# Kernel tuning notes

Hardware: AMD Instinct MI355X
Metric: run time of the kernel (lower is better)

## Reference

```python
import jax, jax.numpy as jnp
import numpy as np

T_STEPS = 10       # T_pos = T_neg = 10 hardcoded in forward
ATTN_SCALE = 0.125 # scale hardcoded in forward (not head_dim**-0.5)
V_TH = 1.0         # spikingjelly IFNode defaults: v_threshold=1.0, v_reset=0.0 (hard reset)
SG_ALPHA = 4.0     # default Sigmoid surrogate alpha

@jax.custom_vjp
def spike(v):
    return (v >= 0.0).astype(v.dtype)

def _spike_fwd(v):
    return spike(v), v

def _spike_bwd(v, g):
    sg = jax.nn.sigmoid(SG_ALPHA * v)
    return (g * SG_ALPHA * sg * (1.0 - sg),)

spike.defvjp(_spike_fwd, _spike_bwd)

def if_node_const_input(y, T=T_STEPS):
    """Multi-step IF neuron driven by the SAME input y at every step.
    charge: v += y; fire: s = H(v - 1); hard reset: v = (1 - s) * v.
    Returns spikes of shape [T, *y.shape]."""
    def step(v, _):
        v = v + y
        s = spike(v - V_TH)
        v = (1.0 - s) * v
        return v, s
    _, spikes = jax.lax.scan(step, jnp.zeros_like(y), None, length=T)
    return spikes

def setup_inputs() -> dict:
    key = jax.random.key(0)
    ks = jax.random.split(key, 6)
    N, C = 2048, 2048
    x = jax.random.normal(ks[0], (N, C), dtype=jnp.float32)
    freqs_cis = jax.random.normal(ks[1], (N, 64), dtype=jnp.float32)  # unused by forward
    w_scale = 0.02
    wq = jax.random.normal(ks[2], (C, C), dtype=jnp.float32) * w_scale
    wk = jax.random.normal(ks[3], (C, C), dtype=jnp.float32) * w_scale
    wv = jax.random.normal(ks[4], (C, C), dtype=jnp.float32) * w_scale
    wo = jax.random.normal(ks[5], (C, C), dtype=jnp.float32) * w_scale
    return {"x": x, "freqs_cis": freqs_cis, "wq": wq, "wk": wk, "wv": wv, "wo": wo}

def reference(x, freqs_cis, wq, wk, wv, wo):
    N, C = x.shape
    n_heads, head_dim = 16, 128  # C == n_heads * head_dim; n_kv_heads == n_heads so repeat_kv is a no-op
    T = T_STEPS

    x_pos = jax.nn.relu(x)
    x_neg = jax.nn.relu(-x)

    # Input is identical at every timestep, so apply the linear once, then run IF over T.
    def branch(xb):
        q = if_node_const_input(xb @ wq)  # [T, N, C] binary spikes
        k = if_node_const_input(xb @ wk)
        v = if_node_const_input(xb @ wv)
        return q, k, v

    qp, kp, vp = branch(x_pos)
    qn, kn, vn = branch(x_neg)
    xq = (qp - qn).reshape(T, N, n_heads, head_dim)
    xk = (kp - kn).reshape(T, N, n_heads, head_dim)
    xv = (vp - vn).reshape(T, N, n_heads, head_dim)

    # no-softmax attention over the HEAD axis, per token: [T,N,H,H]
    attn = jnp.einsum('tnhd,tnmd->tnhm', xq, xk) * ATTN_SCALE
    x_attn = jnp.einsum('tnhm,tnmd->tnhd', attn, xv)          # [T,N,H,Dh]
    x_attn = jnp.swapaxes(x_attn, -1, -2).reshape(T, N, C)    # transpose(-1,-2) then merge

    xo = x_attn @ wo  # [T, N, C]
    return xo.mean(axis=0)
```

## Files before the change

kernel.cpp:

```cpp
#include <hip/hip_runtime.h>
#include <hip/hip_bf16.h>


#define LIST_CAP (512u * 1024u)
#define FLAG_EPS 4e-4f

typedef __attribute__((ext_vector_type(8))) short short8;
typedef __attribute__((ext_vector_type(16))) float floatx16;

__device__ const unsigned d_LUT[16] = {0u, 0x3FFu, 0x2AAu, 0x124u, 0x88u,
                                       0x210u, 0x20u, 0x40u, 0x80u, 0x100u,
                                       0x200u, 0u, 0u, 0u, 0u, 0u};

__device__ __forceinline__ void bf16x2_rne(float a, unsigned& p1, unsigned& p2) {
  const unsigned u = __float_as_uint(a);
  const unsigned t1 = u + 0x7FFFu + ((u >> 16) & 1u);
  p1 = t1 >> 16;
  const float r = a - __uint_as_float(t1 & 0xFFFF0000u);
  const unsigned u2 = __float_as_uint(r);
  p2 = (u2 + 0x7FFFu + ((u2 >> 16) & 1u)) >> 16;
}

template <int ZERO_CNT, int FRAG>
__global__ __launch_bounds__(256) void wsplit(
    const float* __restrict__ W0, const float* __restrict__ W1,
    const float* __restrict__ W2, unsigned short* __restrict__ Bpk,
    int NCT, unsigned* __restrict__ cnt) {
  if (ZERO_CNT && blockIdx.x == 0 && blockIdx.y == 0 && threadIdx.x == 0)
    *cnt = 0u;
  __shared__ float Wf[32 * 132];
  const int ct = blockIdx.x, k0 = blockIdx.y * 32;
  const int c0 = ct * 128;
  const int sel = c0 >> 11;
  const float* W = (sel == 0) ? W0 : ((sel == 1) ? W1 : W2);
  const int cc0 = c0 & 2047;
  const int t = threadIdx.x;

  const int kr = t >> 3, cq = (t & 7) * 16;
#pragma unroll
  for (int u = 0; u < 4; u++) {
    const float4 v = *(const float4*)(W + (size_t)(k0 + kr) * 2048 + cc0 + cq + 4 * u);
    *(float4*)&Wf[kr * 132 + cq + 4 * u] = v;
  }
  __syncthreads();

  const int cc = t >> 1, ch0 = (t & 1) * 2;
  if (FRAG) {
    unsigned short* base = Bpk + ((size_t)((ct >> 1) * 64 + blockIdx.y)) * 16384 +
                           (size_t)(ct & 1) * 8192;
#pragma unroll
    for (int c = ch0; c < ch0 + 2; c++) {
      unsigned q1[8], q2[8];
#pragma unroll
      for (int e = 0; e < 8; e++) bf16x2_rne(Wf[(c * 8 + e) * 132 + cc], q1[e], q2[e]);
      const int ks = c >> 1, kh = c & 1;
      const int off1 = ((0 * 2 + ks) * 4 + (cc >> 5)) * 512 + (kh * 32 + (cc & 31)) * 8;
      const int off2 = ((1 * 2 + ks) * 4 + (cc >> 5)) * 512 + (kh * 32 + (cc & 31)) * 8;
      uint4 P1, P2;
      P1.x = q1[0] | (q1[1] << 16); P1.y = q1[2] | (q1[3] << 16);
      P1.z = q1[4] | (q1[5] << 16); P1.w = q1[6] | (q1[7] << 16);
      P2.x = q2[0] | (q2[1] << 16); P2.y = q2[2] | (q2[3] << 16);
      P2.z = q2[4] | (q2[5] << 16); P2.w = q2[6] | (q2[7] << 16);
      *(uint4*)&base[off1] = P1;
      *(uint4*)&base[off2] = P2;
    }
  } else {
    unsigned short* img1 = Bpk + ((size_t)(0 * NCT + ct) * 64 + blockIdx.y) * 4096;
    unsigned short* img2 = Bpk + ((size_t)(1 * NCT + ct) * 64 + blockIdx.y) * 4096;
#pragma unroll
    for (int c = ch0; c < ch0 + 2; c++) {
      unsigned q1[8], q2[8];
#pragma unroll
      for (int e = 0; e < 8; e++) bf16x2_rne(Wf[(c * 8 + e) * 132 + cc], q1[e], q2[e]);
      const int off = cc * 32 + 8 * (c ^ ((cc >> 1) & 3));
      uint4 P1, P2;
      P1.x = q1[0] | (q1[1] << 16); P1.y = q1[2] | (q1[3] << 16);
      P1.z = q1[4] | (q1[5] << 16); P1.w = q1[6] | (q1[7] << 16);
      P2.x = q2[0] | (q2[1] << 16); P2.y = q2[2] | (q2[3] << 16);
      P2.z = q2[4] | (q2[5] << 16); P2.w = q2[6] | (q2[7] << 16);
      *(uint4*)&img1[off] = P1;
      *(uint4*)&img2[off] = P2;
    }
  }
}

template <int RELU, int FRAG>
__global__ __launch_bounds__(256) void asplit(
    const float* __restrict__ src, unsigned short* __restrict__ Apk, int NRT) {
  const int rt = blockIdx.x, k0i = blockIdx.y;
  const int t = threadIdx.x;
  const int r = t >> 1, half = t & 1;
  int grow = rt * 128 + r;
  float sgn = 1.f;
  if (RELU && grow >= 2048) { grow -= 2048; sgn = -1.f; }
  const float* s = src + (size_t)grow * 2048 + k0i * 32 + half * 16;
  float f[16];
#pragma unroll
  for (int u = 0; u < 4; u++) {
    const float4 v = *(const float4*)(s + 4 * u);
    f[4 * u + 0] = v.x; f[4 * u + 1] = v.y;
    f[4 * u + 2] = v.z; f[4 * u + 3] = v.w;
  }
  if (RELU) {
#pragma unroll
    for (int e = 0; e < 16; e++) f[e] = fmaxf(sgn * f[e], 0.f);
  }
  unsigned q1[16], q2[16];
#pragma unroll
  for (int e = 0; e < 16; e++) bf16x2_rne(f[e], q1[e], q2[e]);

  if (FRAG) {
    unsigned short* base = Apk + ((size_t)((rt >> 1) * 64 + k0i)) * 16384 +
                           (size_t)(rt & 1) * 8192;
#pragma unroll
    for (int cc = 0; cc < 2; cc++) {
      const int c = half * 2 + cc;
      const int ks = c >> 1, kh = c & 1;
      const int off1 = ((0 * 2 + ks) * 4 + (r >> 5)) * 512 + (kh * 32 + (r & 31)) * 8;
      const int off2 = ((1 * 2 + ks) * 4 + (r >> 5)) * 512 + (kh * 32 + (r & 31)) * 8;
      const int e0 = cc * 8;
      uint4 P1, P2;
      P1.x = q1[e0 + 0] | (q1[e0 + 1] << 16); P1.y = q1[e0 + 2] | (q1[e0 + 3] << 16);
      P1.z = q1[e0 + 4] | (q1[e0 + 5] << 16); P1.w = q1[e0 + 6] | (q1[e0 + 7] << 16);
      P2.x = q2[e0 + 0] | (q2[e0 + 1] << 16); P2.y = q2[e0 + 2] | (q2[e0 + 3] << 16);
      P2.z = q2[e0 + 4] | (q2[e0 + 5] << 16); P2.w = q2[e0 + 6] | (q2[e0 + 7] << 16);
      *(uint4*)&base[off1] = P1;
      *(uint4*)&base[off2] = P2;
    }
  } else {
    unsigned short* img1 = Apk + ((size_t)(0 * NRT + rt) * 64 + k0i) * 4096;
    unsigned short* img2 = Apk + ((size_t)(1 * NRT + rt) * 64 + k0i) * 4096;
#pragma unroll
    for (int cc = 0; cc < 2; cc++) {
      const int c = half * 2 + cc;
      const int off = r * 32 + 8 * (c ^ ((r >> 1) & 3));
      const int e0 = cc * 8;
      uint4 P1, P2;
      P1.x = q1[e0 + 0] | (q1[e0 + 1] << 16); P1.y = q1[e0 + 2] | (q1[e0 + 3] << 16);
      P1.z = q1[e0 + 4] | (q1[e0 + 5] << 16); P1.w = q1[e0 + 6] | (q1[e0 + 7] << 16);
      P2.x = q2[e0 + 0] | (q2[e0 + 1] << 16); P2.y = q2[e0 + 2] | (q2[e0 + 3] << 16);
      P2.z = q2[e0 + 4] | (q2[e0 + 5] << 16); P2.w = q2[e0 + 6] | (q2[e0 + 7] << 16);
      *(uint4*)&img1[off] = P1;
      *(uint4*)&img2[off] = P2;
    }
  }
}

__global__ __launch_bounds__(512, 2) void gemm256(
    const unsigned short* __restrict__ Apk, const unsigned short* __restrict__ Bpk,
    unsigned char* __restrict__ MaskJ, unsigned* __restrict__ list,
    unsigned* __restrict__ cnt) {
  __shared__ unsigned short lds[2][4][8192];

  const int tid = threadIdx.x;
  const int wave = tid >> 6, lane = tid & 63;
  const int lm = lane & 31, lg = lane >> 5;
  const int wr = wave >> 2, wc = wave & 3;

  const int orig = (int)blockIdx.x;
  const int wg = (orig & 7) * 48 + (orig >> 3);
  const int bx = wg % 24, by = wg / 24;

  const unsigned short* Aimg = Apk + (size_t)by * 64 * 16384;
  const unsigned short* Bimg = Bpk + (size_t)bx * 64 * 16384;

  auto issue2 = [&](int kt, int nb, int c) {
    const unsigned short* g = ((c < 2) ? (Aimg + (size_t)c * 8192)
                                       : (Bimg + (size_t)(c - 2) * 8192)) +
                              (size_t)kt * 16384;
#pragma unroll
    for (int rr = 0; rr < 2; rr++)
      __builtin_amdgcn_global_load_lds(
          (const __attribute__((address_space(1))) unsigned*)(g + rr * 4096 + tid * 8),
          (__attribute__((address_space(3))) unsigned*)(&lds[nb][c][rr * 4096 + wave * 512]),
          16, 0, 0);
  };

  floatx16 acc[4][2];
#pragma unroll
  for (int i = 0; i < 4; i++)
#pragma unroll
    for (int j = 0; j < 2; j++)
#pragma unroll
      for (int e = 0; e < 16; e++) acc[i][j][e] = 0.f;

#pragma unroll
  for (int c = 0; c < 4; c++) issue2(0, 0, c);
  asm volatile("s_waitcnt vmcnt(0)" ::: "memory");
  __builtin_amdgcn_s_barrier();
  __builtin_amdgcn_sched_barrier(0);

  const int rt0 = 2 * (wc & 1);
  for (int kt = 0; kt < 64; kt++) {
    const int cur = kt & 1, nxt = cur ^ 1;
    const unsigned short* Ab = &lds[cur][wr][0];
    const unsigned short* Bb = &lds[cur][2 + (wc >> 1)][0];
#pragma unroll
    for (int ks = 0; ks < 2; ks++) {
      short8 a1[4], a2[4];
#pragma unroll
      for (int it = 0; it < 4; it++) {
        a1[it] = *(const short8*)&Ab[((0 * 2 + ks) * 4 + it) * 512 + lane * 8];
        a2[it] = *(const short8*)&Ab[((1 * 2 + ks) * 4 + it) * 512 + lane * 8];
      }
#pragma unroll
      for (int jt = 0; jt < 2; jt++) {
        const short8 b1 = *(const short8*)&Bb[((0 * 2 + ks) * 4 + rt0 + jt) * 512 + lane * 8];
        const short8 b2 = *(const short8*)&Bb[((1 * 2 + ks) * 4 + rt0 + jt) * 512 + lane * 8];
        if (ks == 0 && kt < 63) {
          issue2(kt + 1, nxt, jt * 2 + 0);
          issue2(kt + 1, nxt, jt * 2 + 1);
        }
        __builtin_amdgcn_s_barrier();
        __builtin_amdgcn_s_setprio(1);
#pragma unroll
        for (int it = 0; it < 4; it++)
          acc[it][jt] = __builtin_amdgcn_mfma_f32_32x32x16_bf16(a1[it], b1, acc[it][jt], 0, 0, 0);
#pragma unroll
        for (int it = 0; it < 4; it++)
          acc[it][jt] = __builtin_amdgcn_mfma_f32_32x32x16_bf16(a1[it], b2, acc[it][jt], 0, 0, 0);
#pragma unroll
        for (int it = 0; it < 4; it++)
          acc[it][jt] = __builtin_amdgcn_mfma_f32_32x32x16_bf16(a2[it], b1, acc[it][jt], 0, 0, 0);
        __builtin_amdgcn_s_setprio(0);
        if (ks == 1 && jt == 1)
          asm volatile("s_waitcnt vmcnt(0)" ::: "memory");
        __builtin_amdgcn_s_barrier();
      }
    }
    __builtin_amdgcn_sched_barrier(0);
  }

#pragma unroll
  for (int it = 0; it < 4; it++) {
#pragma unroll
    for (int jt = 0; jt < 2; jt++) {
      const int gn = bx * 256 + 64 * wc + 32 * jt + lm;
#pragma unroll
      for (int reg = 0; reg < 16; reg++) {
        const int gm = by * 256 + 128 * wr + 32 * it + (reg & 3) + 8 * (reg >> 2) + 4 * lg;
        const float y = acc[it][jt][reg];
        float r = __builtin_amdgcn_rcpf(y);
        r = fminf(fmaxf(r, -1.0f), 12.0f);
        const float jf = floorf(r);
        const float d0 = fmaf(jf, y, -1.0f);
        const float i0 = fminf(fmaxf(jf, 1.0f), 10.0f);
        const float i1 = fminf(fmaxf(jf + 1.0f, 1.0f), 10.0f);
        const float e0 = fmaf(i0, y, -1.0f);
        const float e1 = fmaf(i1, y, -1.0f);
        const float mind = fminf(fabsf(e0), fabsf(e1));
        const unsigned J = (unsigned)(int)((d0 >= 0.0f) ? jf : jf + 1.0f);
        MaskJ[(size_t)gm * 6144 + gn] = (unsigned char)((J <= 10u) ? J : 0u);
        if (mind < FLAG_EPS) {
          const unsigned idx = atomicAdd(cnt, 1u);
          if (idx < LIST_CAP) list[idx] = ((unsigned)gm << 13) | (unsigned)gn;
        }
      }
    }
  }
}

template <int MODE>
__global__ __launch_bounds__(256, 4) void gemm_dma(
    const unsigned short* __restrict__ Apk, const unsigned short* __restrict__ Bpk,
    int NRT, int NCT, unsigned char* __restrict__ MaskJ,
    unsigned* __restrict__ list, unsigned* __restrict__ cnt,
    float* __restrict__ Out) {
  __shared__ unsigned short sh[4][4096];

  const int tid = threadIdx.x;
  const int bx = blockIdx.x, by = blockIdx.y;
  const int lane = tid & 63, wave = tid >> 6;
  const int wr = wave >> 1, wc = wave & 1;
  const int lm = lane & 31, lg = lane >> 5;

  const unsigned short* gsrc =
      (wave < 2) ? (Apk + ((size_t)(wave * NRT + by) * 64) * 4096)
                 : (Bpk + ((size_t)((wave - 2) * NCT + bx) * 64) * 4096);

  floatx16 acc[2][2];
#pragma unroll
  for (int i = 0; i < 2; i++)
#pragma unroll
    for (int j = 0; j < 2; j++)
#pragma unroll
      for (int e = 0; e < 16; e++) acc[i][j][e] = 0.f;

  for (int k0i = 0; k0i < 64; k0i++) {
    __syncthreads();
    const unsigned short* gp = gsrc + (size_t)k0i * 4096;
#pragma unroll
    for (int i = 0; i < 8; i++) {
      __builtin_amdgcn_global_load_lds(
          (const __attribute__((address_space(1))) unsigned*)(gp + i * 512 + lane * 8),
          (__attribute__((address_space(3))) unsigned*)(&sh[wave][i * 512]), 16, 0, 0);
    }
    __syncthreads();

#pragma unroll
    for (int ks = 0; ks < 2; ks++) {
      const int ch = ks * 2 + lg;
      short8 a1[2], a2[2], b1[2], b2[2];
#pragma unroll
      for (int it = 0; it < 2; it++) {
        const int row = 64 * wr + 32 * it + lm;
        const int off = row * 32 + 8 * (ch ^ ((row >> 1) & 3));
        a1[it] = *(const short8*)&sh[0][off];
        a2[it] = *(const short8*)&sh[1][off];
      }
#pragma unroll
      for (int jt = 0; jt < 2; jt++) {
        const int row = 64 * wc + 32 * jt + lm;
        const int off = row * 32 + 8 * (ch ^ ((row >> 1) & 3));
        b1[jt] = *(const short8*)&sh[2][off];
        b2[jt] = *(const short8*)&sh[3][off];
      }
#pragma unroll
      for (int it = 0; it < 2; it++)
#pragma unroll
        for (int jt = 0; jt < 2; jt++)
          acc[it][jt] = __builtin_amdgcn_mfma_f32_32x32x16_bf16(
              a1[it], b1[jt], acc[it][jt], 0, 0, 0);
#pragma unroll
      for (int it = 0; it < 2; it++)
#pragma unroll
        for (int jt = 0; jt < 2; jt++)
          acc[it][jt] = __builtin_amdgcn_mfma_f32_32x32x16_bf16(
              a1[it], b2[jt], acc[it][jt], 0, 0, 0);
#pragma unroll
      for (int it = 0; it < 2; it++)
#pragma unroll
        for (int jt = 0; jt < 2; jt++)
          acc[it][jt] = __builtin_amdgcn_mfma_f32_32x32x16_bf16(
              a2[it], b1[jt], acc[it][jt], 0, 0, 0);
    }
  }

#pragma unroll
  for (int it = 0; it < 2; it++) {
#pragma unroll
    for (int jt = 0; jt < 2; jt++) {
      const int gn = bx * 128 + 64 * wc + 32 * jt + lm;
#pragma unroll
      for (int reg = 0; reg < 16; reg++) {
        const int gm = by * 128 + 64 * wr + 32 * it + (reg & 3) + 8 * (reg >> 2) + 4 * lg;
        const float y = acc[it][jt][reg];
        if (MODE == 1) {
          Out[(size_t)gm * 2048 + gn] = y * 0.1f;
        } else {
          float r = __builtin_amdgcn_rcpf(y);
          r = fminf(fmaxf(r, -1.0f), 12.0f);
          const float jf = floorf(r);
          const float d0 = fmaf(jf, y, -1.0f);
          const float i0 = fminf(fmaxf(jf, 1.0f), 10.0f);
          const float i1 = fminf(fmaxf(jf + 1.0f, 1.0f), 10.0f);
          const float e0 = fmaf(i0, y, -1.0f);
          const float e1 = fmaf(i1, y, -1.0f);
          const float mind = fminf(fabsf(e0), fabsf(e1));
          const unsigned J = (unsigned)(int)((d0 >= 0.0f) ? jf : jf + 1.0f);
          MaskJ[(size_t)gm * 6144 + gn] = (unsigned char)((J <= 10u) ? J : 0u);
          if (mind < FLAG_EPS) {
            const unsigned idx = atomicAdd(cnt, 1u);
            if (idx < LIST_CAP) list[idx] = ((unsigned)gm << 13) | (unsigned)gn;
          }
        }
      }
    }
  }
}

__global__ __launch_bounds__(256) void transpose_w(
    const float* __restrict__ W0, const float* __restrict__ W1,
    const float* __restrict__ W2, float* __restrict__ WT) {
  __shared__ float tile[32][33];
  const int k0 = blockIdx.x * 32;
  const int c0 = blockIdx.y * 32;
  const int sel = c0 >> 11;
  const float* W = (sel == 0) ? W0 : ((sel == 1) ? W1 : W2);
  const int cc0 = c0 & 2047;
  const int tx = threadIdx.x, ty = threadIdx.y;
#pragma unroll
  for (int rep = 0; rep < 4; rep++)
    tile[ty + 8 * rep][tx] = W[(size_t)(k0 + ty + 8 * rep) * 2048 + cc0 + tx];
  __syncthreads();
#pragma unroll
  for (int rep = 0; rep < 4; rep++)
    WT[(size_t)(c0 + ty + 8 * rep) * 2048 + k0 + tx] = tile[tx][ty + 8 * rep];
}

__global__ __launch_bounds__(256) void rescue(
    const float* __restrict__ X, const float* __restrict__ WT,
    const unsigned* __restrict__ list, const unsigned* __restrict__ cnt,
    unsigned char* __restrict__ MaskJ) {
  const unsigned nItems = min(*cnt, LIST_CAP);
  const unsigned gtid = blockIdx.x * blockDim.x + threadIdx.x;
  const unsigned wave = gtid >> 6, lane = gtid & 63;
  const unsigned nWaves = (gridDim.x * blockDim.x) >> 6;

  for (unsigned i = wave; i < nItems; i += nWaves) {
    const unsigned e = list[i];
    const int r = (int)(e >> 13), c = (int)(e & 8191u);
    const float* xrow = X + (size_t)((r < 2048) ? r : r - 2048) * 2048;
    const float sg = (r < 2048) ? 1.f : -1.f;
    const float* wrow = WT + (size_t)c * 2048;
    double s = 0.0;
#pragma unroll
    for (int it = 0; it < 8; it++) {
      const int k = (it * 64 + (int)lane) * 4;
      const float4 xv = *(const float4*)(xrow + k);
      const float4 wv = *(const float4*)(wrow + k);
      const float a0 = fmaxf(sg * xv.x, 0.f);
      const float a1 = fmaxf(sg * xv.y, 0.f);
      const float a2 = fmaxf(sg * xv.z, 0.f);
      const float a3 = fmaxf(sg * xv.w, 0.f);
      s += (double)a0 * (double)wv.x + (double)a1 * (double)wv.y +
           (double)a2 * (double)wv.z + (double)a3 * (double)wv.w;
    }
#pragma unroll
    for (int off = 32; off > 0; off >>= 1) s += __shfl_down(s, off);
    if (lane == 0) {
      double v = 0.0;
      unsigned J = 0;
#pragma unroll
      for (int t = 0; t < 10; t++) {
        v += s;
        if (J == 0u && v >= 1.0) J = (unsigned)(t + 1);
      }
      MaskJ[(size_t)r * 6144 + c] = (unsigned char)J;
    }
  }
}

__global__ __launch_bounds__(256) void spike_attn(const unsigned char* __restrict__ MaskJ,
                                                  float* __restrict__ xbar) {
  const int n = blockIdx.x;
  const int tid = threadIdx.x;
  const int lane = tid & 63;

  __shared__ unsigned long long qpB[16][2], qnB[16][2], kpB[16][2], knB[16][2];
  __shared__ float xvT[16 * 132];
  __shared__ float attnS[16 * 17];
  __shared__ unsigned lutS[16];

  if (tid < 16) lutS[tid] = d_LUT[tid];
  __syncthreads();

  const unsigned char* mp = MaskJ + (size_t)n * 6144;
  const unsigned char* mn = MaskJ + (size_t)(n + 2048) * 6144;

  unsigned q_p[8], q_n[8], k_p[8], k_n[8], v_p[8], v_n[8];
#pragma unroll
  for (int j = 0; j < 8; j++) {
    const int c = tid + 256 * j;
    q_p[j] = lutS[mp[c]];        q_n[j] = lutS[mn[c]];
    k_p[j] = lutS[mp[2048 + c]]; k_n[j] = lutS[mn[2048 + c]];
    v_p[j] = lutS[mp[4096 + c]]; v_n[j] = lutS[mn[4096 + c]];
  }

  float acc[8];
#pragma unroll
  for (int j = 0; j < 8; j++) acc[j] = 0.f;

  for (int t = 0; t < 10; t++) {
#pragma unroll
    for (int j = 0; j < 8; j++) {
      const int c = tid + 256 * j;
      const unsigned long long bqp = __ballot((q_p[j] >> t) & 1u);
      const unsigned long long bqn = __ballot((q_n[j] >> t) & 1u);
      const unsigned long long bkp = __ballot((k_p[j] >> t) & 1u);
      const unsigned long long bkn = __ballot((k_n[j] >> t) & 1u);
      const int h = c >> 7, word = (c >> 6) & 1;
      if (lane == 0) {
        qpB[h][word] = bqp; qnB[h][word] = bqn;
        kpB[h][word] = bkp; knB[h][word] = bkn;
      }
      const int m = h, d = c & 127;
      xvT[m * 132 + d] =
          (float)((v_p[j] >> t) & 1u) - (float)((v_n[j] >> t) & 1u);
    }
    __syncthreads();

    {
      const int h = tid >> 4, m = tid & 15;
      int dot = 0;
#pragma unroll
      for (int w = 0; w < 2; w++) {
        const unsigned long long qp = qpB[h][w], qn = qnB[h][w];
        const unsigned long long kp = kpB[m][w], kn = knB[m][w];
        dot += __popcll(qp & kp) + __popcll(qn & kn) -
               __popcll(qp & kn) - __popcll(qn & kp);
      }
      attnS[h * 17 + m] = (float)dot * 0.125f;
    }
    __syncthreads();

    {
      const int h = tid & 15;
      float arow[16];
#pragma unroll
      for (int m = 0; m < 16; m++) arow[m] = attnS[h * 17 + m];
#pragma unroll
      for (int j = 0; j < 8; j++) {
        const int d = (tid + 256 * j) >> 4;
        float s = 0.f;
#pragma unroll
        for (int m = 0; m < 16; m++) s += arow[m] * xvT[m * 132 + d];
        acc[j] += s;
      }
    }
    __syncthreads();
  }

#pragma unroll
  for (int j = 0; j < 8; j++) xbar[(size_t)n * 2048 + tid + 256 * j] = acc[j];
}

extern "C" void kernel_launch(void* const* d_in, const int* in_sizes, int n_in,
                              void* d_out, int out_size, void* d_ws, size_t ws_size,
                              hipStream_t stream) {
  const float* x = (const float*)d_in[0];
  const float* wq = (const float*)d_in[2];
  const float* wk = (const float*)d_in[3];
  const float* wv = (const float*)d_in[4];
  const float* wo = (const float*)d_in[5];
  float* out = (float*)d_out;

  char* ws = (char*)d_ws;
  unsigned char* MaskJ = (unsigned char*)ws;
  unsigned short* WOpk = (unsigned short*)ws;
  char* reg2 = ws + (size_t)4096 * 6144;
  unsigned short* Bpk = (unsigned short*)reg2;
  float* WT = (float*)reg2;
  unsigned short* Xbpk = (unsigned short*)reg2;
  char* reg3 = reg2 + (size_t)6144 * 2048 * 2 * 2;
  unsigned short* Apk = (unsigned short*)reg3;
  float* xbar = (float*)reg3;
  unsigned* list = (unsigned*)(reg3 + (size_t)4096 * 2048 * 2 * 2);
  unsigned* cnt = list + LIST_CAP;

  wsplit<1, 1><<<dim3(48, 64), 256, 0, stream>>>(wq, wk, wv, Bpk, 48, cnt);
  asplit<1, 1><<<dim3(32, 64), 256, 0, stream>>>(x, Apk, 32);
  gemm256<<<384, 512, 0, stream>>>(Apk, Bpk, MaskJ, list, cnt);
  transpose_w<<<dim3(64, 192), dim3(32, 8), 0, stream>>>(wq, wk, wv, WT);
  rescue<<<2048, 256, 0, stream>>>(x, WT, list, cnt, MaskJ);
  spike_attn<<<2048, 256, 0, stream>>>(MaskJ, xbar);
  wsplit<0, 0><<<dim3(16, 64), 256, 0, stream>>>(wo, wo, wo, WOpk, 16, nullptr);
  asplit<0, 0><<<dim3(16, 64), 256, 0, stream>>>(xbar, Xbpk, 16);
  gemm_dma<1><<<dim3(16, 16), 256, 0, stream>>>(Xbpk, WOpk, 16, 16, nullptr, nullptr, nullptr, out);
}
```

Measured before the change: 893.3 us.

## Software-pipeline LDS fragment reads against MFMAs with register double-buffering

```diff
diff --git a/kernel.cpp b/kernel.cpp
--- a/kernel.cpp
+++ b/kernel.cpp
@@ -19,6 +19,51 @@
   const float r = a - __uint_as_float(t1 & 0xFFFF0000u);
   const unsigned u2 = __float_as_uint(r);
   p2 = (u2 + 0x7FFFu + ((u2 >> 16) & 1u)) >> 16;
+}
+
+__device__ __forceinline__ unsigned lds_addr32(const void* p) {
+  return (unsigned)(size_t)(const __attribute__((address_space(3))) char*)p;
+}
+
+__device__ __forceinline__ short8 ds_read_b128a(unsigned addr) {
+  short8 r;
+  asm volatile("ds_read_b128 %0, %1" : "=v"(r) : "v"(addr));
+  return r;
+}
+
+__device__ __forceinline__ void read_set(short8 (&sa1)[4], short8 (&sa2)[4],
+                                         short8 (&sb1)[2], short8 (&sb2)[2],
+                                         unsigned abase, unsigned bbase,
+                                         int rt0, int ks) {
+#pragma unroll
+  for (int it = 0; it < 4; it++) {
+    sa1[it] = ds_read_b128a(abase + (unsigned)((ks * 4 + it) * 1024));
+    sa2[it] = ds_read_b128a(abase + (unsigned)(((2 + ks) * 4 + it) * 1024));
+  }
+#pragma unroll
+  for (int j = 0; j < 2; j++) {
+    sb1[j] = ds_read_b128a(bbase + (unsigned)((ks * 4 + rt0 + j) * 1024));
+    sb2[j] = ds_read_b128a(bbase + (unsigned)(((2 + ks) * 4 + rt0 + j) * 1024));
+  }
+}
+
+__device__ __forceinline__ void mfma_set(floatx16 (&acc)[4][2],
+                                         const short8 (&sa1)[4], const short8 (&sa2)[4],
+                                         const short8 (&sb1)[2], const short8 (&sb2)[2]) {
+  __builtin_amdgcn_s_setprio(1);
+#pragma unroll
+  for (int jt = 0; jt < 2; jt++) {
+#pragma unroll
+    for (int it = 0; it < 4; it++)
+      acc[it][jt] = __builtin_amdgcn_mfma_f32_32x32x16_bf16(sa1[it], sb1[jt], acc[it][jt], 0, 0, 0);
+#pragma unroll
+    for (int it = 0; it < 4; it++)
+      acc[it][jt] = __builtin_amdgcn_mfma_f32_32x32x16_bf16(sa1[it], sb2[jt], acc[it][jt], 0, 0, 0);
+#pragma unroll
+    for (int it = 0; it < 4; it++)
+      acc[it][jt] = __builtin_amdgcn_mfma_f32_32x32x16_bf16(sa2[it], sb1[jt], acc[it][jt], 0, 0, 0);
+  }
+  __builtin_amdgcn_s_setprio(0);
 }
 
 template <int ZERO_CNT, int FRAG>
@@ -164,16 +209,19 @@
   const unsigned short* Aimg = Apk + (size_t)by * 64 * 16384;
   const unsigned short* Bimg = Bpk + (size_t)bx * 64 * 16384;
 
-  auto issue2 = [&](int kt, int nb, int c) {
-    const unsigned short* g = ((c < 2) ? (Aimg + (size_t)c * 8192)
-                                       : (Bimg + (size_t)(c - 2) * 8192)) +
-                              (size_t)kt * 16384;
-#pragma unroll
-    for (int rr = 0; rr < 2; rr++)
-      __builtin_amdgcn_global_load_lds(
-          (const __attribute__((address_space(1))) unsigned*)(g + rr * 4096 + tid * 8),
-          (__attribute__((address_space(3))) unsigned*)(&lds[nb][c][rr * 4096 + wave * 512]),
-          16, 0, 0);
+  auto stage = [&](int kt, int nb) {
+#pragma unroll
+    for (int c = 0; c < 4; c++) {
+      const unsigned short* g = ((c < 2) ? (Aimg + (size_t)c * 8192)
+                                         : (Bimg + (size_t)(c - 2) * 8192)) +
+                                (size_t)kt * 16384;
+#pragma unroll
+      for (int rr = 0; rr < 2; rr++)
+        __builtin_amdgcn_global_load_lds(
+            (const __attribute__((address_space(1))) unsigned*)(g + rr * 4096 + tid * 8),
+            (__attribute__((address_space(3))) unsigned*)(&lds[nb][c][rr * 4096 + wave * 512]),
+            16, 0, 0);
+    }
   };
 
   floatx16 acc[4][2];
@@ -184,50 +232,47 @@
 #pragma unroll
       for (int e = 0; e < 16; e++) acc[i][j][e] = 0.f;
 
-#pragma unroll
-  for (int c = 0; c < 4; c++) issue2(0, 0, c);
+  const int rt0 = 2 * (wc & 1);
+  const unsigned laneByte = (unsigned)(lane * 16);
+  const unsigned aB0 = lds_addr32(&lds[0][wr][0]) + laneByte;
+  const unsigned aB1 = lds_addr32(&lds[1][wr][0]) + laneByte;
+  const unsigned bB0 = lds_addr32(&lds[0][2 + (wc >> 1)][0]) + laneByte;
+  const unsigned bB1 = lds_addr32(&lds[1][2 + (wc >> 1)][0]) + laneByte;
+
+  short8 a1A[4], a2A[4], b1A[2], b2A[2];
+  short8 a1B[4], a2B[4], b1B[2], b2B[2];
+
+  stage(0, 0);
   asm volatile("s_waitcnt vmcnt(0)" ::: "memory");
   __builtin_amdgcn_s_barrier();
   __builtin_amdgcn_sched_barrier(0);
-
-  const int rt0 = 2 * (wc & 1);
+  stage(1, 1);
+  read_set(a1A, a2A, b1A, b2A, aB0, bB0, rt0, 0);
+  asm volatile("s_waitcnt lgkmcnt(0)" ::: "memory");
+  __builtin_amdgcn_sched_barrier(0);
+
   for (int kt = 0; kt < 64; kt++) {
-    const int cur = kt & 1, nxt = cur ^ 1;
-    const unsigned short* Ab = &lds[cur][wr][0];
-    const unsigned short* Bb = &lds[cur][2 + (wc >> 1)][0];
-#pragma unroll
-    for (int ks = 0; ks < 2; ks++) {
-      short8 a1[4], a2[4];
-#pragma unroll
-      for (int it = 0; it < 4; it++) {
-        a1[it] = *(const short8*)&Ab[((0 * 2 + ks) * 4 + it) * 512 + lane * 8];
-        a2[it] = *(const short8*)&Ab[((1 * 2 + ks) * 4 + it) * 512 + lane * 8];
-      }
-#pragma unroll
-      for (int jt = 0; jt < 2; jt++) {
-        const short8 b1 = *(const short8*)&Bb[((0 * 2 + ks) * 4 + rt0 + jt) * 512 + lane * 8];
-        const short8 b2 = *(const short8*)&Bb[((1 * 2 + ks) * 4 + rt0 + jt) * 512 + lane * 8];
-        if (ks == 0 && kt < 63) {
-          issue2(kt + 1, nxt, jt * 2 + 0);
-          issue2(kt + 1, nxt, jt * 2 + 1);
-        }
-        __builtin_amdgcn_s_barrier();
-        __builtin_amdgcn_s_setprio(1);
-#pragma unroll
-        for (int it = 0; it < 4; it++)
-          acc[it][jt] = __builtin_amdgcn_mfma_f32_32x32x16_bf16(a1[it], b1, acc[it][jt], 0, 0, 0);
-#pragma unroll
-        for (int it = 0; it < 4; it++)
-          acc[it][jt] = __builtin_amdgcn_mfma_f32_32x32x16_bf16(a1[it], b2, acc[it][jt], 0, 0, 0);
-#pragma unroll
-        for (int it = 0; it < 4; it++)
-          acc[it][jt] = __builtin_amdgcn_mfma_f32_32x32x16_bf16(a2[it], b1, acc[it][jt], 0, 0, 0);
-        __builtin_amdgcn_s_setprio(0);
-        if (ks == 1 && jt == 1)
-          asm volatile("s_waitcnt vmcnt(0)" ::: "memory");
-        __builtin_amdgcn_s_barrier();
-      }
-    }
+    const int cur = kt & 1;
+    const unsigned aCur = cur ? aB1 : aB0;
+    const unsigned bCur = cur ? bB1 : bB0;
+    const unsigned aNxt = cur ? aB0 : aB1;
+    const unsigned bNxt = cur ? bB0 : bB1;
+
+    read_set(a1B, a2B, b1B, b2B, aCur, bCur, rt0, 1);
+    mfma_set(acc, a1A, a2A, b1A, b2A);
+    asm volatile("s_waitcnt lgkmcnt(0)" ::: "memory");
+    __builtin_amdgcn_sched_barrier(0);
+
+    if (kt < 63) {
+      asm volatile("s_waitcnt vmcnt(0)" ::: "memory");
+      __builtin_amdgcn_s_barrier();
+      __builtin_amdgcn_sched_barrier(0);
+      if (kt < 62) stage(kt + 2, cur);
+      read_set(a1A, a2A, b1A, b2A, aNxt, bNxt, rt0, 0);
+    }
+
+    mfma_set(acc, a1B, a2B, b1B, b2B);
+    asm volatile("s_waitcnt lgkmcnt(0)" ::: "memory");
     __builtin_amdgcn_sched_barrier(0);
   }
 
```

Result: no change. 894.7 us (+0.2%).
